# Kernel optimization log

Measured on AMD Instinct MI355X. Metric: run time of the kernel, lower is better.

## Reference

```python
import jax, jax.numpy as jnp
import numpy as np

ALPHA = (0.02, 0.04, 0.08, 0.16)
CHAMFER_W, SMOOTH_W, CURVATURE_W = 1.0, 1.0, 0.3
NS = (8192, 4096, 2048, 1024)
B = 2


def _sqdist(a, b):
    # a: [B,N,3], b: [B,M,3] -> [B,N,M] squared euclidean distance
    return (jnp.sum(a * a, axis=-1)[:, :, None]
            - 2.0 * jnp.einsum('bnc,bmc->bnm', a, b)
            + jnp.sum(b * b, axis=-1)[:, None, :])


def _knn(d, k):
    # k smallest distances + indices along last axis
    neg, idx = jax.lax.top_k(-d, k)
    return -neg, idx


def _gather(points, idx):
    # points: [B,M,C], idx: [B,N,K] -> [B,N,K,C]
    return jax.vmap(lambda p, i: p[i])(points, idx)


def _scale_loss(pc1, pc2, flow):
    # pc1, pc2, flow: [B,3,N]-like -> permute to points-last layout
    p1 = jnp.transpose(pc1, (0, 2, 1))   # [B,N,3]
    p2 = jnp.transpose(pc2, (0, 2, 1))   # [B,M,3]
    fl = jnp.transpose(flow, (0, 2, 1))  # [B,N,3]
    warp = p1 + fl                        # warped pc1

    # curvature of pc2 (10-NN on pc2 itself)
    _, k22 = _knn(_sqdist(p2, p2), 10)
    cv2 = jnp.sum(_gather(p2, k22) - p2[:, :, None, :], axis=2) / 9.0  # [B,M,3]

    # 10-NN on pc1 (shared for warped curvature and smoothness; 9-NN is prefix)
    _, k11 = _knn(_sqdist(p1, p1), 10)
    cvw = jnp.sum(_gather(warp, k11) - warp[:, :, None, :], axis=2) / 9.0  # [B,N,3]

    k9 = k11[:, :, :9]
    gfl = _gather(fl, k9)  # [B,N,9,3]
    smooth = jnp.sum(jnp.linalg.norm(gfl - fl[:, :, None, :], axis=3), axis=2) / 8.0  # [B,N]

    # chamfer between warped pc1 and pc2
    d12 = _sqdist(warp, p2)               # [B,N,M]
    dist1 = jnp.min(d12, axis=-1)         # [B,N]
    dist2 = jnp.min(d12, axis=1)          # [B,M]

    # inverse-distance interpolation of pc2 curvature onto warped pc1 (5-NN)
    dist, kidx = _knn(d12, 5)             # [B,N,5]
    gcv = _gather(cv2, kidx)              # [B,N,5,3]
    w = 1.0 / (dist + 1e-8)
    w = w / jnp.sum(w, axis=2, keepdims=True)
    inter = jnp.sum(w[..., None] * gcv, axis=2)  # [B,N,3]

    chamfer = jnp.mean(jnp.sum(dist1, axis=1)) + jnp.mean(jnp.sum(dist2, axis=1))
    smoothness = jnp.mean(jnp.sum(smooth, axis=1))
    curv = jnp.mean(jnp.sum(jnp.sum((inter - cvw) ** 2, axis=2), axis=1))
    return chamfer, smoothness, curv


def setup_inputs() -> dict:
    key = jax.random.key(0)
    keys = jax.random.split(key, 12)
    out = {}
    names = ['pc1', 'pc2', 'flow']
    k = 0
    for name in names:
        for i, n in enumerate(NS):
            scale = 1.0 if name != 'flow' else 0.1
            out[f'{name}_{i}'] = scale * jax.random.normal(keys[k], (B, 3, n), dtype=jnp.float32)
            k += 1
    return out


def reference(pc1_0, pc1_1, pc1_2, pc1_3,
              pc2_0, pc2_1, pc2_2, pc2_3,
              flow_0, flow_1, flow_2, flow_3):
    pcs1 = (pc1_0, pc1_1, pc1_2, pc1_3)
    pcs2 = (pc2_0, pc2_1, pc2_2, pc2_3)
    flows = (flow_0, flow_1, flow_2, flow_3)
    ch = sm = cv = jnp.float32(0.0)
    for a, p1, p2, fl in zip(ALPHA, pcs1, pcs2, flows):
        c, s, k = _scale_loss(p1, p2, fl)
        ch = ch + a * c
        sm = sm + a * s
        cv = cv + a * k
    total = CHAMFER_W * ch + CURVATURE_W * cv + SMOOTH_W * sm
    return jnp.reshape(total, (1,))
```

## Files before the change

kernel.cpp:

```cpp
#include <hip/hip_runtime.h>
#include <math.h>


#define UNIT 1024
#define NTOT 15360
#define MASKC 0xFFFFE000u
#define NTASK 2380u

typedef unsigned int uint;
typedef __attribute__((ext_vector_type(16))) float f16v;

struct Params {
  const float* pc1[4];
  const float* pc2[4];
  const float* fl[4];
  float4* cv2;
  float4* cvw;
  float* keys;
  uint* d2u;
  uint* cnt;
  float* warp;
  float* out;
};


__device__ __forceinline__ float wave_sum(float v) {
  #pragma unroll
  for (int o = 32; o; o >>= 1) v += __shfl_down(v, o, 64);
  return v;
}

template <int K>
__device__ __forceinline__ void key_insert(float (&kd)[K], float kf) {
  #pragma unroll
  for (int m = K - 1; m >= 1; --m)
    kd[m] = __builtin_amdgcn_fmed3f(kf, kd[m - 1], kd[m]);
  kd[0] = fminf(kd[0], kf);
}

template <int K>
__device__ __forceinline__ void merge_pair(float (&a)[K], const float (&b)[K]) {
  #pragma unroll
  for (int m = 0; m < K; ++m) key_insert<K>(a, b[m]);
}

__device__ __forceinline__ float pack_key_u(float d, uint iw) {
  return __uint_as_float((__float_as_uint(d) & MASKC) | iw);
}

__device__ __forceinline__ void sload3x16(const float* px, const float* py,
                                          const float* pz, int boff,
                                          f16v& x, f16v& y, f16v& z) {
  asm volatile(
      "s_load_dwordx16 %0, %3, %6\n\t"
      "s_load_dwordx16 %1, %4, %6\n\t"
      "s_load_dwordx16 %2, %5, %6\n\t"
      "s_waitcnt lgkmcnt(0)"
      : "=&s"(x), "=&s"(y), "=&s"(z)
      : "s"(px), "s"(py), "s"(pz), "s"(boff));
}

template <int K>
__device__ void scan_k(const float* px, const float* py, const float* pz,
                       int lo, float ax, float ay, float az,
                       float (&a)[K], float (&b)[K]) {
  #pragma unroll 1
  for (int c0 = 0; c0 < UNIT; c0 += 16) {
    f16v xs, ys, zs;
    sload3x16(px, py, pz, (lo + c0) * 4, xs, ys, zs);
    #pragma unroll
    for (int t = 0; t < 16; t += 2) {
      float dxa = xs[t] - ax, dya = ys[t] - ay, dza = zs[t] - az;
      float dA = fmaf(dxa, dxa, fmaf(dya, dya, dza * dza));
      float dxb = xs[t + 1] - ax, dyb = ys[t + 1] - ay, dzb = zs[t + 1] - az;
      float dB = fmaf(dxb, dxb, fmaf(dyb, dyb, dzb * dzb));
      key_insert<K>(a, pack_key_u(dA, (uint)(lo + c0 + t)));
      key_insert<K>(b, pack_key_u(dB, (uint)(lo + c0 + t + 1)));
    }
  }
}

__device__ void scan_m(const float* px, const float* py, const float* pz,
                       int lo, int len, float ax, float ay, float az,
                       float& a0, float& b0) {
  #pragma unroll 1
  for (int c0 = 0; c0 < len; c0 += 16) {
    f16v xs, ys, zs;
    sload3x16(px, py, pz, (lo + c0) * 4, xs, ys, zs);
    #pragma unroll
    for (int t = 0; t < 16; t += 2) {
      float dxa = xs[t] - ax, dya = ys[t] - ay, dza = zs[t] - az;
      float dA = fmaf(dxa, dxa, fmaf(dya, dya, dza * dza));
      float dxb = xs[t + 1] - ax, dyb = ys[t + 1] - ay, dzb = zs[t + 1] - az;
      float dB = fmaf(dxb, dxb, fmaf(dyb, dyb, dzb * dzb));
      a0 = fminf(a0, dA);
      b0 = fminf(b0, dB);
    }
  }
}

__device__ __forceinline__ void decode(int r, int wv, int& s, int& b,
                                       int& i0, int& lo, int& N, int& cpw,
                                       int& off, float& alpha) {
  int rr;
  if (r < 256)      { s = 0; rr = r; }
  else if (r < 320) { s = 1; rr = r - 256; }
  else if (r < 336) { s = 2; rr = r - 320; }
  else              { s = 3; rr = r - 336; }
  N = 8192 >> s;
  cpw = 8 >> s;
  int perb = 128 >> (2 * s);
  b = rr >> (7 - 2 * s);
  int chunk = rr & (perb - 1);
  int qg = (chunk << s) + (wv >> (3 - s));
  i0 = qg << 6;
  lo = (wv & (cpw - 1)) << 10;
  off = 16384 - (16384 >> s);
  alpha = 0.02f * (float)(1 << s);
}

template <int K>
__device__ __forceinline__ bool merge_group(float (&a)[K], float* sm,
                                            int tid, int cpw) {
  const int STR = K | 1;
  int q = tid & 63, wv = tid >> 6;
  #pragma unroll
  for (int m = 0; m < K; ++m) sm[(wv * 64 + q) * STR + m] = a[m];
  __syncthreads();
  if (wv & (cpw - 1)) return false;
  for (int w = wv + 1; w < wv + cpw; ++w)
    #pragma unroll
    for (int m = 0; m < K; ++m)
      key_insert<K>(a, sm[(w * 64 + q) * STR + m]);
  return true;
}


__global__ __launch_bounds__(256) void k_init(Params P) {
  int t = blockIdx.x * 256 + threadIdx.x;
  if (t == 0) { P.out[0] = 0.f; *P.cnt = 1024u; }
  if (t < 2 * NTOT) P.d2u[t] = 0x7F7FFFFFu;
  int s, r;
  if (t < 49152)      { s = 0; r = t; }
  else if (t < 73728) { s = 1; r = t - 49152; }
  else if (t < 86016) { s = 2; r = t - 73728; }
  else if (t < 92160) { s = 3; r = t - 86016; }
  else return;
  int base6 = (s == 0) ? 0 : (s == 1) ? 49152 : (s == 2) ? 73728 : 86016;
  P.warp[base6 + r] = P.pc1[s][r] + P.fl[s][r];
}

__global__ __launch_bounds__(512, 8) void k_work(Params P) {
  __shared__ float sm[8 * 64 * 11];
  __shared__ uint ts;
  int tid = threadIdx.x, q = tid & 63, wv = tid >> 6;

  uint t = blockIdx.x;
  while (t < NTASK) {
    if (t < 1020u) {
      int pass = (int)t / 340, r = (int)t % 340;
      int s, b, i0, lo, N, cpw, off; float alpha;
      decode(r, wv, s, b, i0, lo, N, cpw, off, alpha);
      int i = i0 + q;
      int lo_u = __builtin_amdgcn_readfirstlane(lo);

      if (pass == 0) {
        const float* p2 = P.pc2[s] + b * 3 * N;
        float ax = p2[i], ay = p2[N + i], az = p2[2 * N + i];
        float a[10], bb[10];
        #pragma unroll
        for (int m = 0; m < 10; ++m) { a[m] = 3.0e38f; bb[m] = 3.0e38f; }
        scan_k<10>(p2, p2 + N, p2 + 2 * N, lo_u, ax, ay, az, a, bb);
        merge_pair<10>(a, bb);
        if (merge_group<10>(a, sm, tid, cpw)) {
          float sx = 0.f, sy = 0.f, sz = 0.f;
          #pragma unroll
          for (int m = 0; m < 10; ++m) {
            int j = (int)(__float_as_uint(a[m]) & 0x1FFFu);
            sx += p2[j]; sy += p2[N + j]; sz += p2[2 * N + j];
          }
          const float inv9 = 1.f / 9.f;
          P.cv2[b * NTOT + off + i] = make_float4((sx - 10.f * ax) * inv9,
                                                  (sy - 10.f * ay) * inv9,
                                                  (sz - 10.f * az) * inv9,
                                                  0.f);
        }
      } else if (pass == 1) {
        const float* p1 = P.pc1[s] + b * 3 * N;
        const float* fl = P.fl[s] + b * 3 * N;
        float ax = p1[i], ay = p1[N + i], az = p1[2 * N + i];
        float a[10], bb[10];
        #pragma unroll
        for (int m = 0; m < 10; ++m) { a[m] = 3.0e38f; bb[m] = 3.0e38f; }
        scan_k<10>(p1, p1 + N, p1 + 2 * N, lo_u, ax, ay, az, a, bb);
        merge_pair<10>(a, bb);
        if (merge_group<10>(a, sm, tid, cpw)) {
          float fix = fl[i], fiy = fl[N + i], fiz = fl[2 * N + i];
          float wix = ax + fix, wiy = ay + fiy, wiz = az + fiz;
          float sx = 0.f, sy = 0.f, sz = 0.f, smooth = 0.f;
          float dmax = -1.f, worst = 0.f;
          #pragma unroll
          for (int m = 0; m < 10; ++m) {
            int j = (int)(__float_as_uint(a[m]) & 0x1FFFu);
            float px = p1[j], py = p1[N + j], pz = p1[2 * N + j];
            float flx = fl[j], fly = fl[N + j], flz = fl[2 * N + j];
            sx += px + flx; sy += py + fly; sz += pz + flz;
            float ddx = px - ax, ddy = py - ay, ddz = pz - az;
            float d = fmaf(ddx, ddx, fmaf(ddy, ddy, ddz * ddz));
            float gx = flx - fix, gy = fly - fiy, gz = flz - fiz;
            float term = sqrtf(fmaf(gx, gx, fmaf(gy, gy, gz * gz)));
            smooth += term;
            if (d > dmax) { dmax = d; worst = term; }
          }
          smooth -= worst;
          const float inv9 = 1.f / 9.f;
          P.cvw[b * NTOT + off + i] = make_float4((sx - 10.f * wix) * inv9,
                                                  (sy - 10.f * wiy) * inv9,
                                                  (sz - 10.f * wiz) * inv9,
                                                  0.f);
          float ssum = wave_sum(smooth * (1.f / 8.f));
          if (q == 0) atomicAdd(P.out, alpha * 0.5f * ssum);
        }
      } else {
        int base6 = (s == 0) ? 0 : (s == 1) ? 49152 : (s == 2) ? 73728
                                                               : 86016;
        const float* wq = P.warp + base6 + b * 3 * N;
        const float* p2 = P.pc2[s] + b * 3 * N;
        float ax = wq[i], ay = wq[N + i], az = wq[2 * N + i];
        float a[5], bb[5];
        #pragma unroll
        for (int m = 0; m < 5; ++m) { a[m] = 3.0e38f; bb[m] = 3.0e38f; }
        scan_k<5>(p2, p2 + N, p2 + 2 * N, lo_u, ax, ay, az, a, bb);
        merge_pair<5>(a, bb);
        if (merge_group<5>(a, sm, tid, cpw)) {
          #pragma unroll
          for (int m = 0; m < 5; ++m)
            P.keys[m * (2 * NTOT) + b * NTOT + off + i] = a[m];
        }
      }
    } else {
      int dm = (int)(t - 1020u);
      int s, tb;
      if (dm < 1024)      { s = 0; tb = dm; }
      else if (dm < 1280) { s = 1; tb = dm - 1024; }
      else if (dm < 1344) { s = 2; tb = dm - 1280; }
      else                { s = 3; tb = dm - 1344; }
      int N = 8192 >> s;
      int tpb = 512 >> (2 * s);
      int b = tb >> (9 - 2 * s);
      int ti = tb & (tpb - 1);
      int u = ti * 8 + wv;
      int rpq = 32 >> s;
      int qg = u >> (5 - s);
      int rg = u & (rpq - 1);
      int i = qg * 64 + q, lo = rg * 256;
      int off = 16384 - (16384 >> s);
      int base6 = (s == 0) ? 0 : (s == 1) ? 49152 : (s == 2) ? 73728
                                                             : 86016;
      const float* wc = P.warp + base6 + b * 3 * N;
      const float* p2 = P.pc2[s] + b * 3 * N;
      float ax = p2[i], ay = p2[N + i], az = p2[2 * N + i];
      float a0 = 3.0e38f, b0 = 3.0e38f;
      int lo_u = __builtin_amdgcn_readfirstlane(lo);
      scan_m(wc, wc + N, wc + 2 * N, lo_u, 256, ax, ay, az, a0, b0);
      atomicMin(P.d2u + b * NTOT + off + i, __float_as_uint(fminf(a0, b0)));
    }
    __syncthreads();
    if (tid == 0) ts = atomicAdd(P.cnt, 1u);
    __syncthreads();
    t = ts;
  }
}

__global__ __launch_bounds__(256) void k_epi(Params P) {
  int t = blockIdx.x * 256 + threadIdx.x;
  int b = t >= NTOT;
  int r = t - b * NTOT;
  int s, i;
  if (r < 8192)       { s = 0; i = r; }
  else if (r < 12288) { s = 1; i = r - 8192; }
  else if (r < 14336) { s = 2; i = r - 12288; }
  else                { s = 3; i = r - 14336; }
  int N = 8192 >> s;
  int off = 16384 - (16384 >> s);
  float alpha = 0.02f * (float)(1 << s);
  const float* p1 = P.pc1[s] + b * 3 * N;
  const float* fl = P.fl[s] + b * 3 * N;
  const float* p2 = P.pc2[s] + b * 3 * N;
  float ax = p1[i] + fl[i], ay = p1[N + i] + fl[N + i],
        az = p1[2 * N + i] + fl[2 * N + i];
  float dist1 = 3.0e38f, wsum = 0.f, ix = 0.f, iy = 0.f, iz = 0.f;
  #pragma unroll
  for (int m = 0; m < 5; ++m) {
    uint key = __float_as_uint(P.keys[m * (2 * NTOT) + b * NTOT + off + i]);
    int j = (int)(key & 0x1FFFu);
    float px = p2[j], py = p2[N + j], pz = p2[2 * N + j];
    float ddx = px - ax, ddy = py - ay, ddz = pz - az;
    float d = fmaf(ddx, ddx, fmaf(ddy, ddy, ddz * ddz));
    dist1 = fminf(dist1, d);
    float w = 1.f / (d + 1e-8f);
    wsum += w;
    float4 cv = P.cv2[b * NTOT + off + j];
    ix += w * cv.x; iy += w * cv.y; iz += w * cv.z;
  }
  float inv = 1.f / wsum;
  ix *= inv; iy *= inv; iz *= inv;
  float4 cw = P.cvw[b * NTOT + off + i];
  float ex = ix - cw.x, ey = iy - cw.y, ez = iz - cw.z;
  float curv = fmaf(ex, ex, fmaf(ey, ey, ez * ez));
  float csum = wave_sum(dist1 + 0.3f * curv);
  float msum = wave_sum(__uint_as_float(P.d2u[t]));
  if ((threadIdx.x & 63) == 0) {
    atomicAdd(P.out, alpha * 0.5f * csum);
    atomicAdd(P.out, alpha * 0.5f * msum);
  }
}

extern "C" void kernel_launch(void* const* d_in, const int* in_sizes, int n_in,
                              void* d_out, int out_size, void* d_ws,
                              size_t ws_size, hipStream_t stream) {
  Params P;
  for (int s = 0; s < 4; ++s) {
    P.pc1[s] = (const float*)d_in[s];
    P.pc2[s] = (const float*)d_in[4 + s];
    P.fl[s]  = (const float*)d_in[8 + s];
  }
  char* ws = (char*)d_ws;
  P.cv2  = (float4*)ws;
  P.cvw  = (float4*)(ws + 491520);
  P.keys = (float*)(ws + 983040);
  P.d2u  = (uint*)(ws + 1597440);
  P.cnt  = (uint*)(ws + 1720320);
  P.warp = (float*)(ws + 1720384);
  P.out  = (float*)d_out;

  k_init<<<dim3(360), dim3(256), 0, stream>>>(P);
  k_work<<<dim3(1024), dim3(512), 0, stream>>>(P);
  k_epi<<<dim3(120), dim3(256), 0, stream>>>(P);
}
```

Before: 301.9 us.

## Process two query points per thread to reuse scalar-loaded candidate coordinates

Each thread now handles two query points in every kNN and chamfer scan, so each scalar-loaded batch of candidate coordinates feeds twice the distance and insertion work. Task counts, decode mapping, grid size and launch bounds (occupancy 8 to 4 waves) are halved to match, and key packing uses a single v_and_or_b32. This amortizes s_load and loop overhead, at the cost of doubled register pressure for the top-k arrays, lower occupancy and fewer tasks for load balancing.

```diff
diff --git a/kernel.cpp b/kernel.cpp
--- a/kernel.cpp
+++ b/kernel.cpp
@@ -5,7 +5,8 @@
 #define UNIT 1024
 #define NTOT 15360
 #define MASKC 0xFFFFE000u
-#define NTASK 2380u
+#define NHEAVY 510u
+#define NTASK 1190u
 
 typedef unsigned int uint;
 typedef __attribute__((ext_vector_type(16))) float f16v;
@@ -44,10 +45,6 @@
   for (int m = 0; m < K; ++m) key_insert<K>(a, b[m]);
 }
 
-__device__ __forceinline__ float pack_key_u(float d, uint iw) {
-  return __uint_as_float((__float_as_uint(d) & MASKC) | iw);
-}
-
 __device__ __forceinline__ void sload3x16(const float* px, const float* py,
                                           const float* pz, int boff,
                                           f16v& x, f16v& y, f16v& z) {
@@ -60,41 +57,41 @@
       : "s"(px), "s"(py), "s"(pz), "s"(boff));
 }
 
-template <int K>
-__device__ void scan_k(const float* px, const float* py, const float* pz,
-                       int lo, float ax, float ay, float az,
-                       float (&a)[K], float (&b)[K]) {
-  #pragma unroll 1
-  for (int c0 = 0; c0 < UNIT; c0 += 16) {
-    f16v xs, ys, zs;
-    sload3x16(px, py, pz, (lo + c0) * 4, xs, ys, zs);
-    #pragma unroll
-    for (int t = 0; t < 16; t += 2) {
-      float dxa = xs[t] - ax, dya = ys[t] - ay, dza = zs[t] - az;
-      float dA = fmaf(dxa, dxa, fmaf(dya, dya, dza * dza));
-      float dxb = xs[t + 1] - ax, dyb = ys[t + 1] - ay, dzb = zs[t + 1] - az;
-      float dB = fmaf(dxb, dxb, fmaf(dyb, dyb, dzb * dzb));
-      key_insert<K>(a, pack_key_u(dA, (uint)(lo + c0 + t)));
-      key_insert<K>(b, pack_key_u(dB, (uint)(lo + c0 + t + 1)));
-    }
-  }
-}
-
-__device__ void scan_m(const float* px, const float* py, const float* pz,
-                       int lo, int len, float ax, float ay, float az,
-                       float& a0, float& b0) {
+template <int K, bool MIN>
+__device__ void scan2(const float* px, const float* py, const float* pz,
+                      int lo, int len, float ax0, float ay0, float az0,
+                      float ax1, float ay1, float az1, uint vmask,
+                      float (&a0)[K], float (&b0)[K],
+                      float (&a1)[K], float (&b1)[K]) {
   #pragma unroll 1
   for (int c0 = 0; c0 < len; c0 += 16) {
     f16v xs, ys, zs;
     sload3x16(px, py, pz, (lo + c0) * 4, xs, ys, zs);
     #pragma unroll
-    for (int t = 0; t < 16; t += 2) {
-      float dxa = xs[t] - ax, dya = ys[t] - ay, dza = zs[t] - az;
-      float dA = fmaf(dxa, dxa, fmaf(dya, dya, dza * dza));
-      float dxb = xs[t + 1] - ax, dyb = ys[t + 1] - ay, dzb = zs[t + 1] - az;
-      float dB = fmaf(dxb, dxb, fmaf(dyb, dyb, dzb * dzb));
-      a0 = fminf(a0, dA);
-      b0 = fminf(b0, dB);
+    for (int t = 0; t < 16; ++t) {
+      float X = xs[t], Y = ys[t], Z = zs[t];
+      float dx0 = X - ax0, dy0 = Y - ay0, dz0 = Z - az0;
+      float d0 = fmaf(dx0, dx0, fmaf(dy0, dy0, dz0 * dz0));
+      float dx1 = X - ax1, dy1 = Y - ay1, dz1 = Z - az1;
+      float d1 = fmaf(dx1, dx1, fmaf(dy1, dy1, dz1 * dz1));
+      if (MIN) {
+        if (t & 1) { b0[0] = fminf(b0[0], d0); b1[0] = fminf(b1[0], d1); }
+        else       { a0[0] = fminf(a0[0], d0); a1[0] = fminf(a1[0], d1); }
+      } else {
+        uint idx = (uint)(lo + c0 + t);
+        uint k0, k1;
+        asm("v_and_or_b32 %0, %1, %2, %3" : "=v"(k0)
+            : "v"(__float_as_uint(d0)), "v"(vmask), "s"(idx));
+        asm("v_and_or_b32 %0, %1, %2, %3" : "=v"(k1)
+            : "v"(__float_as_uint(d1)), "v"(vmask), "s"(idx));
+        if (t & 1) {
+          key_insert<K>(b0, __uint_as_float(k0));
+          key_insert<K>(b1, __uint_as_float(k1));
+        } else {
+          key_insert<K>(a0, __uint_as_float(k0));
+          key_insert<K>(a1, __uint_as_float(k1));
+        }
+      }
     }
   }
 }
@@ -103,42 +100,42 @@
                                        int& i0, int& lo, int& N, int& cpw,
                                        int& off, float& alpha) {
   int rr;
-  if (r < 256)      { s = 0; rr = r; }
-  else if (r < 320) { s = 1; rr = r - 256; }
-  else if (r < 336) { s = 2; rr = r - 320; }
-  else              { s = 3; rr = r - 336; }
+  if (r < 128)      { s = 0; rr = r; }
+  else if (r < 160) { s = 1; rr = r - 128; }
+  else if (r < 168) { s = 2; rr = r - 160; }
+  else              { s = 3; rr = r - 168; }
   N = 8192 >> s;
   cpw = 8 >> s;
-  int perb = 128 >> (2 * s);
-  b = rr >> (7 - 2 * s);
+  int perb = 64 >> (2 * s);
+  b = rr >> (6 - 2 * s);
   int chunk = rr & (perb - 1);
   int qg = (chunk << s) + (wv >> (3 - s));
-  i0 = qg << 6;
+  i0 = qg << 7;
   lo = (wv & (cpw - 1)) << 10;
   off = 16384 - (16384 >> s);
   alpha = 0.02f * (float)(1 << s);
 }
 
 template <int K>
-__device__ __forceinline__ bool merge_group(float (&a)[K], float* sm,
-                                            int tid, int cpw) {
+__device__ __forceinline__ void merge_slot(float (&a)[K], float* sm,
+                                           int tid, int cpw, bool lead) {
   const int STR = K | 1;
   int q = tid & 63, wv = tid >> 6;
   #pragma unroll
   for (int m = 0; m < K; ++m) sm[(wv * 64 + q) * STR + m] = a[m];
   __syncthreads();
-  if (wv & (cpw - 1)) return false;
-  for (int w = wv + 1; w < wv + cpw; ++w)
-    #pragma unroll
-    for (int m = 0; m < K; ++m)
-      key_insert<K>(a, sm[(w * 64 + q) * STR + m]);
-  return true;
+  if (lead)
+    for (int w = wv + 1; w < wv + cpw; ++w)
+      #pragma unroll
+      for (int m = 0; m < K; ++m)
+        key_insert<K>(a, sm[(w * 64 + q) * STR + m]);
+  __syncthreads();
 }
 
 
 __global__ __launch_bounds__(256) void k_init(Params P) {
   int t = blockIdx.x * 256 + threadIdx.x;
-  if (t == 0) { P.out[0] = 0.f; *P.cnt = 1024u; }
+  if (t == 0) { P.out[0] = 0.f; *P.cnt = 512u; }
   if (t < 2 * NTOT) P.d2u[t] = 0x7F7FFFFFu;
   int s, r;
   if (t < 49152)      { s = 0; r = t; }
@@ -150,75 +147,134 @@
   P.warp[base6 + r] = P.pc1[s][r] + P.fl[s][r];
 }
 
-__global__ __launch_bounds__(512, 8) void k_work(Params P) {
+__global__ __launch_bounds__(512, 4) void k_work(Params P) {
   __shared__ float sm[8 * 64 * 11];
   __shared__ uint ts;
   int tid = threadIdx.x, q = tid & 63, wv = tid >> 6;
+  uint vmask = MASKC;
 
   uint t = blockIdx.x;
   while (t < NTASK) {
-    if (t < 1020u) {
-      int pass = (int)t / 340, r = (int)t % 340;
+    if (t < NHEAVY) {
+      int pass = (int)t / 170, r = (int)t % 170;
       int s, b, i0, lo, N, cpw, off; float alpha;
       decode(r, wv, s, b, i0, lo, N, cpw, off, alpha);
-      int i = i0 + q;
+      int i = i0 + q, i2 = i0 + 64 + q;
       int lo_u = __builtin_amdgcn_readfirstlane(lo);
+      bool lead = (wv & (cpw - 1)) == 0;
 
       if (pass == 0) {
         const float* p2 = P.pc2[s] + b * 3 * N;
-        float ax = p2[i], ay = p2[N + i], az = p2[2 * N + i];
-        float a[10], bb[10];
+        float ax0 = p2[i], ay0 = p2[N + i], az0 = p2[2 * N + i];
+        float ax1 = p2[i2], ay1 = p2[N + i2], az1 = p2[2 * N + i2];
+        float a0[10], b0[10], a1[10], b1[10];
         #pragma unroll
-        for (int m = 0; m < 10; ++m) { a[m] = 3.0e38f; bb[m] = 3.0e38f; }
-        scan_k<10>(p2, p2 + N, p2 + 2 * N, lo_u, ax, ay, az, a, bb);
-        merge_pair<10>(a, bb);
-        if (merge_group<10>(a, sm, tid, cpw)) {
+        for (int m = 0; m < 10; ++m) {
+          a0[m] = 3.0e38f; b0[m] = 3.0e38f;
+          a1[m] = 3.0e38f; b1[m] = 3.0e38f;
+        }
+        scan2<10, false>(p2, p2 + N, p2 + 2 * N, lo_u, UNIT,
+                         ax0, ay0, az0, ax1, ay1, az1, vmask,
+                         a0, b0, a1, b1);
+        merge_pair<10>(a0, b0);
+        merge_pair<10>(a1, b1);
+        merge_slot<10>(a0, sm, tid, cpw, lead);
+        merge_slot<10>(a1, sm, tid, cpw, lead);
+        if (lead) {
+          const float inv9 = 1.f / 9.f;
           float sx = 0.f, sy = 0.f, sz = 0.f;
           #pragma unroll
           for (int m = 0; m < 10; ++m) {
-            int j = (int)(__float_as_uint(a[m]) & 0x1FFFu);
+            int j = (int)(__float_as_uint(a0[m]) & 0x1FFFu);
             sx += p2[j]; sy += p2[N + j]; sz += p2[2 * N + j];
           }
-          const float inv9 = 1.f / 9.f;
-          P.cv2[b * NTOT + off + i] = make_float4((sx - 10.f * ax) * inv9,
-                                                  (sy - 10.f * ay) * inv9,
-                                                  (sz - 10.f * az) * inv9,
+          P.cv2[b * NTOT + off + i] = make_float4((sx - 10.f * ax0) * inv9,
+                                                  (sy - 10.f * ay0) * inv9,
+                                                  (sz - 10.f * az0) * inv9,
                                                   0.f);
+          sx = 0.f; sy = 0.f; sz = 0.f;
+          #pragma unroll
+          for (int m = 0; m < 10; ++m) {
+            int j = (int)(__float_as_uint(a1[m]) & 0x1FFFu);
+            sx += p2[j]; sy += p2[N + j]; sz += p2[2 * N + j];
+          }
+          P.cv2[b * NTOT + off + i2] = make_float4((sx - 10.f * ax1) * inv9,
+                                                   (sy - 10.f * ay1) * inv9,
+                                                   (sz - 10.f * az1) * inv9,
+                                                   0.f);
         }
       } else if (pass == 1) {
         const float* p1 = P.pc1[s] + b * 3 * N;
         const float* fl = P.fl[s] + b * 3 * N;
-        float ax = p1[i], ay = p1[N + i], az = p1[2 * N + i];
-        float a[10], bb[10];
+        float ax0 = p1[i], ay0 = p1[N + i], az0 = p1[2 * N + i];
+        float ax1 = p1[i2], ay1 = p1[N + i2], az1 = p1[2 * N + i2];
+        float a0[10], b0[10], a1[10], b1[10];
         #pragma unroll
-        for (int m = 0; m < 10; ++m) { a[m] = 3.0e38f; bb[m] = 3.0e38f; }
-        scan_k<10>(p1, p1 + N, p1 + 2 * N, lo_u, ax, ay, az, a, bb);
-        merge_pair<10>(a, bb);
-        if (merge_group<10>(a, sm, tid, cpw)) {
-          float fix = fl[i], fiy = fl[N + i], fiz = fl[2 * N + i];
-          float wix = ax + fix, wiy = ay + fiy, wiz = az + fiz;
-          float sx = 0.f, sy = 0.f, sz = 0.f, smooth = 0.f;
-          float dmax = -1.f, worst = 0.f;
-          #pragma unroll
-          for (int m = 0; m < 10; ++m) {
-            int j = (int)(__float_as_uint(a[m]) & 0x1FFFu);
-            float px = p1[j], py = p1[N + j], pz = p1[2 * N + j];
-            float flx = fl[j], fly = fl[N + j], flz = fl[2 * N + j];
-            sx += px + flx; sy += py + fly; sz += pz + flz;
-            float ddx = px - ax, ddy = py - ay, ddz = pz - az;
-            float d = fmaf(ddx, ddx, fmaf(ddy, ddy, ddz * ddz));
-            float gx = flx - fix, gy = fly - fiy, gz = flz - fiz;
-            float term = sqrtf(fmaf(gx, gx, fmaf(gy, gy, gz * gz)));
-            smooth += term;
-            if (d > dmax) { dmax = d; worst = term; }
+        for (int m = 0; m < 10; ++m) {
+          a0[m] = 3.0e38f; b0[m] = 3.0e38f;
+          a1[m] = 3.0e38f; b1[m] = 3.0e38f;
+        }
+        scan2<10, false>(p1, p1 + N, p1 + 2 * N, lo_u, UNIT,
+                         ax0, ay0, az0, ax1, ay1, az1, vmask,
+                         a0, b0, a1, b1);
+        merge_pair<10>(a0, b0);
+        merge_pair<10>(a1, b1);
+        merge_slot<10>(a0, sm, tid, cpw, lead);
+        merge_slot<10>(a1, sm, tid, cpw, lead);
+        float ssum_l = 0.f;
+        if (lead) {
+          const float inv9 = 1.f / 9.f;
+          {
+            float fix = fl[i], fiy = fl[N + i], fiz = fl[2 * N + i];
+            float wix = ax0 + fix, wiy = ay0 + fiy, wiz = az0 + fiz;
+            float sx = 0.f, sy = 0.f, sz = 0.f, smooth = 0.f;
+            float dmax = -1.f, worst = 0.f;
+            #pragma unroll
+            for (int m = 0; m < 10; ++m) {
+              int j = (int)(__float_as_uint(a0[m]) & 0x1FFFu);
+              float px = p1[j], py = p1[N + j], pz = p1[2 * N + j];
+              float flx = fl[j], fly = fl[N + j], flz = fl[2 * N + j];
+              sx += px + flx; sy += py + fly; sz += pz + flz;
+              float ddx = px - ax0, ddy = py - ay0, ddz = pz - az0;
+              float d = fmaf(ddx, ddx, fmaf(ddy, ddy, ddz * ddz));
+              float gx = flx - fix, gy = fly - fiy, gz = flz - fiz;
+              float term = sqrtf(fmaf(gx, gx, fmaf(gy, gy, gz * gz)));
+              smooth += term;
+              if (d > dmax) { dmax = d; worst = term; }
+            }
+            smooth -= worst;
+            P.cvw[b * NTOT + off + i] =
+                make_float4((sx - 10.f * wix) * inv9,
+                            (sy - 10.f * wiy) * inv9,
+                            (sz - 10.f * wiz) * inv9, 0.f);
+            ssum_l += smooth;
           }
-          smooth -= worst;
-          const float inv9 = 1.f / 9.f;
-          P.cvw[b * NTOT + off + i] = make_float4((sx - 10.f * wix) * inv9,
-                                                  (sy - 10.f * wiy) * inv9,
-                                                  (sz - 10.f * wiz) * inv9,
-                                                  0.f);
-          float ssum = wave_sum(smooth * (1.f / 8.f));
+          {
+            float fix = fl[i2], fiy = fl[N + i2], fiz = fl[2 * N + i2];
+            float wix = ax1 + fix, wiy = ay1 + fiy, wiz = az1 + fiz;
+            float sx = 0.f, sy = 0.f, sz = 0.f, smooth = 0.f;
+            float dmax = -1.f, worst = 0.f;
+            #pragma unroll
+            for (int m = 0; m < 10; ++m) {
+              int j = (int)(__float_as_uint(a1[m]) & 0x1FFFu);
+              float px = p1[j], py = p1[N + j], pz = p1[2 * N + j];
+              float flx = fl[j], fly = fl[N + j], flz = fl[2 * N + j];
+              sx += px + flx; sy += py + fly; sz += pz + flz;
+              float ddx = px - ax1, ddy = py - ay1, ddz = pz - az1;
+              float d = fmaf(ddx, ddx, fmaf(ddy, ddy, ddz * ddz));
+              float gx = flx - fix, gy = fly - fiy, gz = flz - fiz;
+              float term = sqrtf(fmaf(gx, gx, fmaf(gy, gy, gz * gz)));
+              smooth += term;
+              if (d > dmax) { dmax = d; worst = term; }
+            }
+            smooth -= worst;
+            P.cvw[b * NTOT + off + i2] =
+                make_float4((sx - 10.f * wix) * inv9,
+                            (sy - 10.f * wiy) * inv9,
+                            (sz - 10.f * wiz) * inv9, 0.f);
+            ssum_l += smooth;
+          }
+          float ssum = wave_sum(ssum_l * (1.f / 8.f));
           if (q == 0) atomicAdd(P.out, alpha * 0.5f * ssum);
         }
       } else {
@@ -226,44 +282,62 @@
                                                                : 86016;
         const float* wq = P.warp + base6 + b * 3 * N;
         const float* p2 = P.pc2[s] + b * 3 * N;
-        float ax = wq[i], ay = wq[N + i], az = wq[2 * N + i];
-        float a[5], bb[5];
+        float ax0 = wq[i], ay0 = wq[N + i], az0 = wq[2 * N + i];
+        float ax1 = wq[i2], ay1 = wq[N + i2], az1 = wq[2 * N + i2];
+        float a0[5], b0[5], a1[5], b1[5];
         #pragma unroll
-        for (int m = 0; m < 5; ++m) { a[m] = 3.0e38f; bb[m] = 3.0e38f; }
-        scan_k<5>(p2, p2 + N, p2 + 2 * N, lo_u, ax, ay, az, a, bb);
-        merge_pair<5>(a, bb);
-        if (merge_group<5>(a, sm, tid, cpw)) {
+        for (int m = 0; m < 5; ++m) {
+          a0[m] = 3.0e38f; b0[m] = 3.0e38f;
+          a1[m] = 3.0e38f; b1[m] = 3.0e38f;
+        }
+        scan2<5, false>(p2, p2 + N, p2 + 2 * N, lo_u, UNIT,
+                        ax0, ay0, az0, ax1, ay1, az1, vmask,
+                        a0, b0, a1, b1);
+        merge_pair<5>(a0, b0);
+        merge_pair<5>(a1, b1);
+        merge_slot<5>(a0, sm, tid, cpw, lead);
+        merge_slot<5>(a1, sm, tid, cpw, lead);
+        if (lead) {
           #pragma unroll
-          for (int m = 0; m < 5; ++m)
-            P.keys[m * (2 * NTOT) + b * NTOT + off + i] = a[m];
+          for (int m = 0; m < 5; ++m) {
+            P.keys[m * (2 * NTOT) + b * NTOT + off + i] = a0[m];
+            P.keys[m * (2 * NTOT) + b * NTOT + off + i2] = a1[m];
+          }
         }
       }
     } else {
-      int dm = (int)(t - 1020u);
+      int dm = (int)(t - NHEAVY);
       int s, tb;
-      if (dm < 1024)      { s = 0; tb = dm; }
-      else if (dm < 1280) { s = 1; tb = dm - 1024; }
-      else if (dm < 1344) { s = 2; tb = dm - 1280; }
-      else                { s = 3; tb = dm - 1344; }
+      if (dm < 512)      { s = 0; tb = dm; }
+      else if (dm < 640) { s = 1; tb = dm - 512; }
+      else if (dm < 672) { s = 2; tb = dm - 640; }
+      else               { s = 3; tb = dm - 672; }
       int N = 8192 >> s;
-      int tpb = 512 >> (2 * s);
-      int b = tb >> (9 - 2 * s);
+      int tpb = 256 >> (2 * s);
+      int b = tb >> (8 - 2 * s);
       int ti = tb & (tpb - 1);
       int u = ti * 8 + wv;
-      int rpq = 32 >> s;
+      int rgc = 32 >> s;
       int qg = u >> (5 - s);
-      int rg = u & (rpq - 1);
-      int i = qg * 64 + q, lo = rg * 256;
+      int rg = u & (rgc - 1);
+      int i = qg * 128 + q, i2 = i + 64, lo = rg * 256;
       int off = 16384 - (16384 >> s);
       int base6 = (s == 0) ? 0 : (s == 1) ? 49152 : (s == 2) ? 73728
                                                              : 86016;
       const float* wc = P.warp + base6 + b * 3 * N;
       const float* p2 = P.pc2[s] + b * 3 * N;
-      float ax = p2[i], ay = p2[N + i], az = p2[2 * N + i];
-      float a0 = 3.0e38f, b0 = 3.0e38f;
+      float ax0 = p2[i], ay0 = p2[N + i], az0 = p2[2 * N + i];
+      float ax1 = p2[i2], ay1 = p2[N + i2], az1 = p2[2 * N + i2];
+      float a0[1], b0[1], a1[1], b1[1];
+      a0[0] = 3.0e38f; b0[0] = 3.0e38f; a1[0] = 3.0e38f; b1[0] = 3.0e38f;
       int lo_u = __builtin_amdgcn_readfirstlane(lo);
-      scan_m(wc, wc + N, wc + 2 * N, lo_u, 256, ax, ay, az, a0, b0);
-      atomicMin(P.d2u + b * NTOT + off + i, __float_as_uint(fminf(a0, b0)));
+      scan2<1, true>(wc, wc + N, wc + 2 * N, lo_u, 256,
+                     ax0, ay0, az0, ax1, ay1, az1, vmask,
+                     a0, b0, a1, b1);
+      atomicMin(P.d2u + b * NTOT + off + i,
+                __float_as_uint(fminf(a0[0], b0[0])));
+      atomicMin(P.d2u + b * NTOT + off + i2,
+                __float_as_uint(fminf(a1[0], b1[0])));
     }
     __syncthreads();
     if (tid == 0) ts = atomicAdd(P.cnt, 1u);
@@ -335,6 +409,6 @@
   P.out  = (float*)d_out;
 
   k_init<<<dim3(360), dim3(256), 0, stream>>>(P);
-  k_work<<<dim3(1024), dim3(512), 0, stream>>>(P);
+  k_work<<<dim3(512), dim3(512), 0, stream>>>(P);
   k_epi<<<dim3(120), dim3(256), 0, stream>>>(P);
 }
```

Measured after the change: 329.6 us. 1.09x slower.

## Fuse epilogue into work kernel via grid-wide atomic barrier

Applied to the files above, without the earlier changes.

Removes the separate epilogue launch. All work-kernel blocks now arrive at a global atomic counter and spin until every block has finished, after which the first 60 blocks compute the epilogue reduction. Each block reduces its partial sums in shared memory before issuing one atomic to the output, instead of two atomics per wave. This saves a kernel launch and the gap between kernels, but depends on all 1024 blocks being resident at the same time, otherwise the spin barrier deadlocks. It also has finished blocks idle while they wait.

```diff
diff --git a/kernel.cpp b/kernel.cpp
--- a/kernel.cpp
+++ b/kernel.cpp
@@ -6,6 +6,7 @@
 #define NTOT 15360
 #define MASKC 0xFFFFE000u
 #define NTASK 2380u
+#define NBLK 1024u
 
 typedef unsigned int uint;
 typedef __attribute__((ext_vector_type(16))) float f16v;
@@ -138,7 +139,7 @@
 
 __global__ __launch_bounds__(256) void k_init(Params P) {
   int t = blockIdx.x * 256 + threadIdx.x;
-  if (t == 0) { P.out[0] = 0.f; *P.cnt = 1024u; }
+  if (t == 0) { P.out[0] = 0.f; P.cnt[0] = NBLK; P.cnt[1] = 0u; }
   if (t < 2 * NTOT) P.d2u[t] = 0x7F7FFFFFu;
   int s, r;
   if (t < 49152)      { s = 0; r = t; }
@@ -270,12 +271,25 @@
     __syncthreads();
     t = ts;
   }
-}
-
-__global__ __launch_bounds__(256) void k_epi(Params P) {
-  int t = blockIdx.x * 256 + threadIdx.x;
-  int b = t >= NTOT;
-  int r = t - b * NTOT;
+
+  if (tid == 0) {
+    __threadfence();
+    __hip_atomic_fetch_add(P.cnt + 1, 1u, __ATOMIC_ACQ_REL,
+                           __HIP_MEMORY_SCOPE_AGENT);
+    uint v;
+    do {
+      v = __hip_atomic_load(P.cnt + 1, __ATOMIC_ACQUIRE,
+                            __HIP_MEMORY_SCOPE_AGENT);
+      if (v < NBLK) __builtin_amdgcn_s_sleep(2);
+    } while (v < NBLK);
+    __threadfence();
+  }
+  __syncthreads();
+
+  if (blockIdx.x >= 60u) return;
+  int it = (int)blockIdx.x * 512 + tid;
+  int b = it >= NTOT;
+  int r = it - b * NTOT;
   int s, i;
   if (r < 8192)       { s = 0; i = r; }
   else if (r < 12288) { s = 1; i = r - 8192; }
@@ -308,11 +322,16 @@
   float4 cw = P.cvw[b * NTOT + off + i];
   float ex = ix - cw.x, ey = iy - cw.y, ez = iz - cw.z;
   float curv = fmaf(ex, ex, fmaf(ey, ey, ez * ez));
-  float csum = wave_sum(dist1 + 0.3f * curv);
-  float msum = wave_sum(__uint_as_float(P.d2u[t]));
-  if ((threadIdx.x & 63) == 0) {
-    atomicAdd(P.out, alpha * 0.5f * csum);
-    atomicAdd(P.out, alpha * 0.5f * msum);
+  float v = alpha * 0.5f * (dist1 + 0.3f * curv)
+          + alpha * 0.5f * __uint_as_float(P.d2u[it]);
+  v = wave_sum(v);
+  if (q == 0) sm[wv] = v;
+  __syncthreads();
+  if (tid == 0) {
+    float tot = 0.f;
+    #pragma unroll
+    for (int m = 0; m < 8; ++m) tot += sm[m];
+    atomicAdd(P.out, tot);
   }
 }
 
@@ -335,6 +354,5 @@
   P.out  = (float*)d_out;
 
   k_init<<<dim3(360), dim3(256), 0, stream>>>(P);
-  k_work<<<dim3(1024), dim3(512), 0, stream>>>(P);
-  k_epi<<<dim3(120), dim3(256), 0, stream>>>(P);
-}
+  k_work<<<dim3(NBLK), dim3(512), 0, stream>>>(P);
+}
```

Result: slower. 641.1 us (+112.3%).
